# Optimization experiments

Hardware: AMD Instinct MI355X
Metric: run time of the kernel (lower is better)

The kernel has to match this reference:

```python
import jax, jax.numpy as jnp
import numpy as np

EMBED_DIM = 768
NUM_HEADS = 12
HEAD_DIM = EMBED_DIM // NUM_HEADS


def setup_inputs() -> dict:
    key = jax.random.key(0)
    ks = jax.random.split(key, 5)
    B, N, D = 8, 1024, EMBED_DIM
    s = 1.0 / np.sqrt(D)
    return {
        "x": jax.random.normal(ks[0], (B, N, D), dtype=jnp.float32),
        "qkv_w": jax.random.uniform(ks[1], (D, 3 * D), jnp.float32, -s, s),  # [in, out]
        "qkv_b": jax.random.uniform(ks[2], (3 * D,), jnp.float32, -s, s),
        "proj_w": jax.random.uniform(ks[3], (D, D), jnp.float32, -s, s),
        "proj_b": jax.random.uniform(ks[4], (D,), jnp.float32, -s, s),
    }


def reference(x, qkv_w, qkv_b, proj_w, proj_b):
    B, N, D = x.shape
    H, Hd = NUM_HEADS, HEAD_DIM
    qkv = x @ qkv_w + qkv_b                          # [B, N, 3D]
    qkv = qkv.reshape(B, N, 3, H, Hd)
    q, k, v = (jnp.moveaxis(qkv, 2, 0)[i].transpose(0, 2, 1, 3) for i in range(3))  # each [B, H, N, Hd]
    scores = jnp.einsum("bhnd,bhmd->bhnm", q, k) / np.sqrt(Hd).astype(x.dtype)
    attn = jax.nn.softmax(scores, axis=-1)           # dropout rate 0.0 -> identity
    out = jnp.einsum("bhnm,bhmd->bhnd", attn, v)     # [B, H, N, Hd]
    out = out.transpose(0, 2, 1, 3).reshape(B, N, D)
    return out @ proj_w + proj_b
```

## Files before the change

### kernel.cpp

```cpp
#include <hip/hip_runtime.h>
#include <hip/hip_bf16.h>

typedef __attribute__((ext_vector_type(8))) short short8;
typedef __attribute__((ext_vector_type(4))) float f32x4;
typedef __attribute__((ext_vector_type(2))) unsigned int uint2v;
typedef unsigned int u32;

#define QSCALE 0.1803368801111204f

__device__ inline ushort f2bf(float f) {
    unsigned int i = __builtin_bit_cast(unsigned int, f);
    unsigned int r = (i + 0x7FFFu + ((i >> 16) & 1u)) >> 16;
    return (ushort)r;
}
__device__ inline u32 pack_bf16(float a, float b) {
    float2 f2; f2.x = a; f2.y = b;
    __hip_bfloat162 h = __float22bfloat162_rn(f2);
    u32 r; __builtin_memcpy(&r, &h, 4);
    return r;
}

__device__ __forceinline__ void gload_lds16(const ushort* g, ushort* l) {
    __builtin_amdgcn_global_load_lds(
        (const __attribute__((address_space(1))) u32*)g,
        (__attribute__((address_space(3))) u32*)l, 16, 0, 0);
}

__global__ __launch_bounds__(256) void convert_f32_bf16(
    const float* __restrict__ in, ushort* __restrict__ outp, int n8)
{
    int idx = blockIdx.x * 256 + threadIdx.x;
    if (idx >= n8) return;
    const float4 u0 = *(const float4*)&in[(size_t)idx * 8];
    const float4 u1 = *(const float4*)&in[(size_t)idx * 8 + 4];
    uint2v a, b;
    a.x = pack_bf16(u0.x, u0.y); a.y = pack_bf16(u0.z, u0.w);
    b.x = pack_bf16(u1.x, u1.y); b.y = pack_bf16(u1.z, u1.w);
    *(uint2v*)&outp[(size_t)idx * 8] = a;
    *(uint2v*)&outp[(size_t)idx * 8 + 4] = b;
}

__global__ __launch_bounds__(256) void transpose_f32_bf16(
    const float* __restrict__ W, ushort* __restrict__ Wt, int K, int N)
{
    __shared__ float tile[32][33];
    const int n0 = blockIdx.x * 32;
    const int k0 = blockIdx.y * 32;
    const int tx = threadIdx.x & 31;
    const int ty = threadIdx.x >> 5;
    for (int i = ty; i < 32; i += 8)
        tile[i][tx] = W[(size_t)(k0 + i) * N + n0 + tx];
    __syncthreads();
    for (int i = ty; i < 32; i += 8)
        Wt[(size_t)(n0 + i) * K + k0 + tx] = f2bf(tile[tx][i]);
}

template <bool OUT_FP32, bool QKV_MODE>
__global__ __launch_bounds__(256) void gemm_bt(
    const ushort* __restrict__ A, const ushort* __restrict__ Bt,
    const float* __restrict__ bias, void* __restrict__ C,
    ushort* __restrict__ Vt, int M, int N, int K, int ldc)
{
    __shared__ __attribute__((aligned(16))) ushort As[128][64];
    __shared__ __attribute__((aligned(16))) ushort Bs[128][64];
    const int tid  = threadIdx.x;
    const int lane = tid & 63;
    const int w    = tid >> 6;
    const int wm   = (w >> 1) * 64;
    const int wn   = (w & 1) * 64;
    const int g    = lane >> 4;
    const int t    = lane & 15;
    const int m0   = blockIdx.y * 128;
    const int n0   = blockIdx.x * 128;

    const int lr = lane >> 3;
    const int pc = lane & 7;

    f32x4 acc[4][4];
#pragma unroll
    for (int i = 0; i < 4; i++)
#pragma unroll
        for (int j = 0; j < 4; j++) acc[i][j] = {0.f, 0.f, 0.f, 0.f};

    const int xorc = t & 7;

    for (int k0 = 0; k0 < K; k0 += 64) {
#pragma unroll
        for (int p = 0; p < 4; p++) {
            const int row = w * 32 + p * 8 + lr;
            const int gc  = pc ^ (row & 7);
            gload_lds16(&A[(size_t)(m0 + row) * K + k0 + gc * 8], &As[w * 32 + p * 8][0]);
            gload_lds16(&Bt[(size_t)(n0 + row) * K + k0 + gc * 8], &Bs[w * 32 + p * 8][0]);
        }
        __syncthreads();
#pragma unroll
        for (int s = 0; s < 2; s++) {
            short8 a[4], b[4];
            const int ca = ((s * 4 + g) ^ xorc) * 8;
#pragma unroll
            for (int i = 0; i < 4; i++)
                a[i] = *(const short8*)&As[wm + i * 16 + t][ca];
#pragma unroll
            for (int j = 0; j < 4; j++)
                b[j] = *(const short8*)&Bs[wn + j * 16 + t][ca];
#pragma unroll
            for (int i = 0; i < 4; i++)
#pragma unroll
                for (int j = 0; j < 4; j++)
                    acc[i][j] = __builtin_amdgcn_mfma_f32_16x16x32_bf16(
                        a[i], b[j], acc[i][j], 0, 0, 0);
        }
        __syncthreads();
    }

#pragma unroll
    for (int j = 0; j < 4; j++) {
        int col = n0 + wn + j * 16 + t;
        float bv = bias[col];
        if (QKV_MODE && col >= 1536) {
            int h = (col - 1536) >> 6, d = col & 63;
#pragma unroll
            for (int i = 0; i < 4; i++) {
                int n = m0 + wm + i * 16 + g * 4;
                int bb = n >> 10, nn = n & 1023;
                uint2v u;
                u.x = pack_bf16(acc[i][j][0] + bv, acc[i][j][1] + bv);
                u.y = pack_bf16(acc[i][j][2] + bv, acc[i][j][3] + bv);
                *(uint2v*)&Vt[(((size_t)bb * 12 + h) * 64 + d) * 1024 + nn] = u;
            }
        } else {
#pragma unroll
            for (int i = 0; i < 4; i++)
#pragma unroll
                for (int r = 0; r < 4; r++) {
                    int row = m0 + wm + i * 16 + g * 4 + r;
                    float val = acc[i][j][r] + bv;
                    if (QKV_MODE && col < 768) val *= QSCALE;
                    if (OUT_FP32) ((float*)C)[(size_t)row * ldc + col] = val;
                    else          ((ushort*)C)[(size_t)row * ldc + col] = f2bf(val);
                }
        }
    }
}

#define PD 72
__global__ __launch_bounds__(256) void attn_kernel(
    const ushort* __restrict__ qk, const ushort* __restrict__ Vt,
    ushort* __restrict__ out)
{
    __shared__ __attribute__((aligned(16))) ushort Ks[2][64][64];
    __shared__ __attribute__((aligned(16))) ushort Vs[2][64][64];
    __shared__ __attribute__((aligned(16))) ushort Ps[4][16][PD];

    const int tid  = threadIdx.x;
    const int lane = tid & 63;
    const int w    = tid >> 6;
    const int g    = lane >> 4;
    const int t    = lane & 15;
    const int q0   = blockIdx.x * 128;
    const int h    = blockIdx.y;
    const int b    = blockIdx.z;

    const int srow = tid >> 3;
    const int pc   = tid & 7;
    const size_t base  = (size_t)b * 1024 * 1536;
    const size_t vbase = ((size_t)b * 12 + h) * 64 * 1024;

    short8 qfrag[2][2];
#pragma unroll
    for (int qf = 0; qf < 2; qf++)
#pragma unroll
        for (int s = 0; s < 2; s++)
            qfrag[qf][s] = *(const short8*)&qk[base +
                (size_t)(q0 + qf * 64 + w * 16 + t) * 1536 + h * 64 + s * 32 + g * 8];

#pragma unroll
    for (int p = 0; p < 2; p++) {
        int r = srow + 32 * p;
        int c = (pc ^ (r & 7)) * 8;
        *(short8*)&Ks[0][r][c] =
            *(const short8*)&qk[base + (size_t)r * 1536 + 768 + h * 64 + pc * 8];
        *(short8*)&Vs[0][r][c] =
            *(const short8*)&Vt[vbase + (size_t)r * 1024 + pc * 8];
    }
    __syncthreads();

    f32x4 o_acc[2][4];
#pragma unroll
    for (int qf = 0; qf < 2; qf++)
#pragma unroll
        for (int j = 0; j < 4; j++) o_acc[qf][j] = {0.f, 0.f, 0.f, 0.f};
    float l_part[2] = {0.f, 0.f};

    for (int kt = 0; kt < 16; kt++) {
        const int cur = kt & 1;

        short8 kpre[2], vpre[2];
        if (kt < 15) {
            const int kb = (kt + 1) * 64;
#pragma unroll
            for (int p = 0; p < 2; p++) {
                int r = srow + 32 * p;
                kpre[p] = *(const short8*)&qk[base + (size_t)(kb + r) * 1536 + 768 + h * 64 + pc * 8];
                vpre[p] = *(const short8*)&Vt[vbase + (size_t)r * 1024 + kb + pc * 8];
            }
        }

        short8 kf[2][4], bv[2][4];
#pragma unroll
        for (int s = 0; s < 2; s++)
#pragma unroll
            for (int j = 0; j < 4; j++) {
                const int row = j * 16 + t;
                const int c = ((s * 4 + g) ^ (t & 7)) * 8;
                kf[s][j] = *(const short8*)&Ks[cur][row][c];
                bv[s][j] = *(const short8*)&Vs[cur][row][c];
            }

#pragma unroll
        for (int qf = 0; qf < 2; qf++) {
            f32x4 s_acc[4];
#pragma unroll
            for (int j = 0; j < 4; j++) s_acc[j] = {0.f, 0.f, 0.f, 0.f};
#pragma unroll
            for (int s = 0; s < 2; s++)
#pragma unroll
                for (int j = 0; j < 4; j++)
                    s_acc[j] = __builtin_amdgcn_mfma_f32_16x16x32_bf16(
                        kf[s][j], qfrag[qf][s], s_acc[j], 0, 0, 0);

#pragma unroll
            for (int j = 0; j < 4; j++) {
                float p0 = exp2f(s_acc[j][0]);
                float p1 = exp2f(s_acc[j][1]);
                float p2 = exp2f(s_acc[j][2]);
                float p3 = exp2f(s_acc[j][3]);
                l_part[qf] += (p0 + p1) + (p2 + p3);
                uint2v u;
                u.x = pack_bf16(p0, p1);
                u.y = pack_bf16(p2, p3);
                *(uint2v*)&Ps[w][t][j * 16 + g * 4] = u;
            }

#pragma unroll
            for (int s = 0; s < 2; s++) {
                short8 a = *(const short8*)&Ps[w][t][s * 32 + g * 8];
#pragma unroll
                for (int j = 0; j < 4; j++)
                    o_acc[qf][j] = __builtin_amdgcn_mfma_f32_16x16x32_bf16(
                        a, bv[s][j], o_acc[qf][j], 0, 0, 0);
            }
        }

        if (kt < 15) {
#pragma unroll
            for (int p = 0; p < 2; p++) {
                int r = srow + 32 * p;
                int c = (pc ^ (r & 7)) * 8;
                *(short8*)&Ks[cur ^ 1][r][c] = kpre[p];
                *(short8*)&Vs[cur ^ 1][r][c] = vpre[p];
            }
        }
        __syncthreads();
    }

#pragma unroll
    for (int qf = 0; qf < 2; qf++) {
        float l_tot = l_part[qf];
        l_tot += __shfl_xor(l_tot, 16);
        l_tot += __shfl_xor(l_tot, 32);
        float il[4];
#pragma unroll
        for (int r = 0; r < 4; r++) il[r] = 1.0f / __shfl(l_tot, g * 4 + r);
#pragma unroll
        for (int r = 0; r < 4; r++) {
            int row = q0 + qf * 64 + w * 16 + g * 4 + r;
#pragma unroll
            for (int j = 0; j < 4; j++)
                out[((size_t)(b * 1024 + row)) * 768 + h * 64 + j * 16 + t] =
                    f2bf(o_acc[qf][j][r] * il[r]);
        }
    }
}

extern "C" void kernel_launch(void* const* d_in, const int* in_sizes, int n_in,
                              void* d_out, int out_size, void* d_ws, size_t ws_size,
                              hipStream_t stream)
{
    const float* x      = (const float*)d_in[0];
    const float* qkv_w  = (const float*)d_in[1];
    const float* qkv_b  = (const float*)d_in[2];
    const float* proj_w = (const float*)d_in[3];
    const float* proj_b = (const float*)d_in[4];
    float* out = (float*)d_out;

    char* ws = (char*)d_ws;
    ushort* Wt1 = (ushort*)ws;
    ushort* Wt2 = Wt1 + (size_t)2304 * 768;
    char*   buf = (char*)(Wt2 + (size_t)768 * 768);

    transpose_f32_bf16<<<dim3(72, 24), 256, 0, stream>>>(qkv_w, Wt1, 768, 2304);
    transpose_f32_bf16<<<dim3(24, 24), 256, 0, stream>>>(proj_w, Wt2, 768, 768);

    const size_t wt_bytes   = ((size_t)2304 * 768 + (size_t)768 * 768) * 2;
    const size_t full_bytes = wt_bytes + (size_t)8192 * 768 * 2
                                       + (size_t)8192 * 1536 * 2
                                       + (size_t)8192 * 768 * 2
                                       + (size_t)8192 * 768 * 2;

    if (ws_size >= full_bytes) {
        ushort* xb    = (ushort*)buf;
        ushort* qkO   = xb + (size_t)8192 * 768;
        ushort* VtO   = qkO + (size_t)8192 * 1536;
        ushort* attnO = VtO + (size_t)8192 * 768;
        convert_f32_bf16<<<dim3(3072), 256, 0, stream>>>(x, xb, 786432);
        gemm_bt<false, true><<<dim3(18, 64), 256, 0, stream>>>(
            xb, Wt1, qkv_b, qkO, VtO, 8192, 2304, 768, 1536);
        attn_kernel<<<dim3(8, 12, 8), 256, 0, stream>>>(qkO, VtO, attnO);
        gemm_bt<true, false><<<dim3(6, 64), 256, 0, stream>>>(
            attnO, Wt2, proj_b, out, nullptr, 8192, 768, 768, 768);
    } else {
        ushort* xbB   = (ushort*)buf;
        ushort* qkB   = xbB + (size_t)1024 * 768;
        ushort* VtB   = qkB + (size_t)1024 * 1536;
        ushort* attnB = VtB + (size_t)1024 * 768;
        for (int b = 0; b < 8; b++) {
            const float* xp = x + (size_t)b * 1024 * 768;
            float* outb = out + (size_t)b * 1024 * 768;
            convert_f32_bf16<<<dim3(384), 256, 0, stream>>>(xp, xbB, 98304);
            gemm_bt<false, true><<<dim3(18, 8), 256, 0, stream>>>(
                xbB, Wt1, qkv_b, qkB, VtB, 1024, 2304, 768, 1536);
            attn_kernel<<<dim3(8, 12, 1), 256, 0, stream>>>(qkB, VtB, attnB);
            gemm_bt<true, false><<<dim3(6, 8), 256, 0, stream>>>(
                attnB, Wt2, proj_b, outb, nullptr, 1024, 768, 768, 768);
        }
    }
}
```

Before: 207.8 us.

## Add 64x128-tile projection GEMM and single-buffer attention K/V LDS with register prefetch

Adds a dedicated output-projection GEMM that uses 64x128 tiles, which doubles the block count from 384 to 768 for better CU fill on the 8192x768 problem. The attention kernel moves from double-buffered K/V shared memory to a single buffer. It prefetches tiles two steps ahead in registers and adds an extra barrier per iteration. This cuts LDS use, which may raise occupancy, but it adds a sync and the prefetch distance changes.

```diff
diff --git a/kernel.cpp b/kernel.cpp
--- a/kernel.cpp
+++ b/kernel.cpp
@@ -143,13 +143,88 @@
     }
 }
 
+__global__ __launch_bounds__(256) void gemm_bt2(
+    const ushort* __restrict__ A, const ushort* __restrict__ Bt,
+    const float* __restrict__ bias, float* __restrict__ C,
+    int M, int N, int K, int ldc)
+{
+    __shared__ __attribute__((aligned(16))) ushort As[64][64];
+    __shared__ __attribute__((aligned(16))) ushort Bs[128][64];
+    const int tid  = threadIdx.x;
+    const int lane = tid & 63;
+    const int w    = tid >> 6;
+    const int g    = lane >> 4;
+    const int t    = lane & 15;
+    const int m0   = blockIdx.y * 64;
+    const int n0   = blockIdx.x * 128;
+    const int wn   = w * 32;
+
+    const int lr = lane >> 3;
+    const int pc = lane & 7;
+
+    f32x4 acc[4][2];
+#pragma unroll
+    for (int i = 0; i < 4; i++)
+#pragma unroll
+        for (int j = 0; j < 2; j++) acc[i][j] = {0.f, 0.f, 0.f, 0.f};
+
+    const int xorc = t & 7;
+
+    for (int k0 = 0; k0 < K; k0 += 64) {
+#pragma unroll
+        for (int p = 0; p < 2; p++) {
+            const int row = w * 16 + p * 8 + lr;
+            const int gc  = pc ^ (row & 7);
+            gload_lds16(&A[(size_t)(m0 + row) * K + k0 + gc * 8], &As[w * 16 + p * 8][0]);
+        }
+#pragma unroll
+        for (int p = 0; p < 4; p++) {
+            const int row = w * 32 + p * 8 + lr;
+            const int gc  = pc ^ (row & 7);
+            gload_lds16(&Bt[(size_t)(n0 + row) * K + k0 + gc * 8], &Bs[w * 32 + p * 8][0]);
+        }
+        __syncthreads();
+#pragma unroll
+        for (int s = 0; s < 2; s++) {
+            short8 a[4], b[2];
+            const int ca = ((s * 4 + g) ^ xorc) * 8;
+#pragma unroll
+            for (int i = 0; i < 4; i++)
+                a[i] = *(const short8*)&As[i * 16 + t][ca];
+#pragma unroll
+            for (int j = 0; j < 2; j++)
+                b[j] = *(const short8*)&Bs[wn + j * 16 + t][ca];
+#pragma unroll
+            for (int i = 0; i < 4; i++)
+#pragma unroll
+                for (int j = 0; j < 2; j++)
+                    acc[i][j] = __builtin_amdgcn_mfma_f32_16x16x32_bf16(
+                        a[i], b[j], acc[i][j], 0, 0, 0);
+        }
+        __syncthreads();
+    }
+
+#pragma unroll
+    for (int j = 0; j < 2; j++) {
+        int col = n0 + wn + j * 16 + t;
+        float bv = bias[col];
+#pragma unroll
+        for (int i = 0; i < 4; i++)
+#pragma unroll
+            for (int r = 0; r < 4; r++) {
+                int row = m0 + i * 16 + g * 4 + r;
+                C[(size_t)row * ldc + col] = acc[i][j][r] + bv;
+            }
+    }
+}
+
 #define PD 72
 __global__ __launch_bounds__(256) void attn_kernel(
     const ushort* __restrict__ qk, const ushort* __restrict__ Vt,
     ushort* __restrict__ out)
 {
-    __shared__ __attribute__((aligned(16))) ushort Ks[2][64][64];
-    __shared__ __attribute__((aligned(16))) ushort Vs[2][64][64];
+    __shared__ __attribute__((aligned(16))) ushort Ks[64][64];
+    __shared__ __attribute__((aligned(16))) ushort Vs[64][64];
     __shared__ __attribute__((aligned(16))) ushort Ps[4][16][PD];
 
     const int tid  = threadIdx.x;
@@ -178,10 +253,17 @@
     for (int p = 0; p < 2; p++) {
         int r = srow + 32 * p;
         int c = (pc ^ (r & 7)) * 8;
-        *(short8*)&Ks[0][r][c] =
+        *(short8*)&Ks[r][c] =
             *(const short8*)&qk[base + (size_t)r * 1536 + 768 + h * 64 + pc * 8];
-        *(short8*)&Vs[0][r][c] =
+        *(short8*)&Vs[r][c] =
             *(const short8*)&Vt[vbase + (size_t)r * 1024 + pc * 8];
+    }
+    short8 kpre[2], vpre[2];
+#pragma unroll
+    for (int p = 0; p < 2; p++) {
+        int r = srow + 32 * p;
+        kpre[p] = *(const short8*)&qk[base + (size_t)(64 + r) * 1536 + 768 + h * 64 + pc * 8];
+        vpre[p] = *(const short8*)&Vt[vbase + (size_t)r * 1024 + 64 + pc * 8];
     }
     __syncthreads();
 
@@ -193,19 +275,6 @@
     float l_part[2] = {0.f, 0.f};
 
     for (int kt = 0; kt < 16; kt++) {
-        const int cur = kt & 1;
-
-        short8 kpre[2], vpre[2];
-        if (kt < 15) {
-            const int kb = (kt + 1) * 64;
-#pragma unroll
-            for (int p = 0; p < 2; p++) {
-                int r = srow + 32 * p;
-                kpre[p] = *(const short8*)&qk[base + (size_t)(kb + r) * 1536 + 768 + h * 64 + pc * 8];
-                vpre[p] = *(const short8*)&Vt[vbase + (size_t)r * 1024 + kb + pc * 8];
-            }
-        }
-
         short8 kf[2][4], bv[2][4];
 #pragma unroll
         for (int s = 0; s < 2; s++)
@@ -213,9 +282,29 @@
             for (int j = 0; j < 4; j++) {
                 const int row = j * 16 + t;
                 const int c = ((s * 4 + g) ^ (t & 7)) * 8;
-                kf[s][j] = *(const short8*)&Ks[cur][row][c];
-                bv[s][j] = *(const short8*)&Vs[cur][row][c];
-            }
+                kf[s][j] = *(const short8*)&Ks[row][c];
+                bv[s][j] = *(const short8*)&Vs[row][c];
+            }
+        __syncthreads();
+
+        if (kt < 15) {
+#pragma unroll
+            for (int p = 0; p < 2; p++) {
+                int r = srow + 32 * p;
+                int c = (pc ^ (r & 7)) * 8;
+                *(short8*)&Ks[r][c] = kpre[p];
+                *(short8*)&Vs[r][c] = vpre[p];
+            }
+            if (kt < 14) {
+                const int kb = (kt + 2) * 64;
+#pragma unroll
+                for (int p = 0; p < 2; p++) {
+                    int r = srow + 32 * p;
+                    kpre[p] = *(const short8*)&qk[base + (size_t)(kb + r) * 1536 + 768 + h * 64 + pc * 8];
+                    vpre[p] = *(const short8*)&Vt[vbase + (size_t)r * 1024 + kb + pc * 8];
+                }
+            }
+        }
 
 #pragma unroll
         for (int qf = 0; qf < 2; qf++) {
@@ -251,16 +340,6 @@
                         a, bv[s][j], o_acc[qf][j], 0, 0, 0);
             }
         }
-
-        if (kt < 15) {
-#pragma unroll
-            for (int p = 0; p < 2; p++) {
-                int r = srow + 32 * p;
-                int c = (pc ^ (r & 7)) * 8;
-                *(short8*)&Ks[cur ^ 1][r][c] = kpre[p];
-                *(short8*)&Vs[cur ^ 1][r][c] = vpre[p];
-            }
-        }
         __syncthreads();
     }
 
@@ -317,8 +396,8 @@
         gemm_bt<false, true><<<dim3(18, 64), 256, 0, stream>>>(
             xb, Wt1, qkv_b, qkO, VtO, 8192, 2304, 768, 1536);
         attn_kernel<<<dim3(8, 12, 8), 256, 0, stream>>>(qkO, VtO, attnO);
-        gemm_bt<true, false><<<dim3(6, 64), 256, 0, stream>>>(
-            attnO, Wt2, proj_b, out, nullptr, 8192, 768, 768, 768);
+        gemm_bt2<<<dim3(6, 128), 256, 0, stream>>>(
+            attnO, Wt2, proj_b, out, 8192, 768, 768, 768);
     } else {
         ushort* xbB   = (ushort*)buf;
         ushort* qkB   = xbB + (size_t)1024 * 768;
@@ -331,8 +410,8 @@
             gemm_bt<false, true><<<dim3(18, 8), 256, 0, stream>>>(
                 xbB, Wt1, qkv_b, qkB, VtB, 1024, 2304, 768, 1536);
             attn_kernel<<<dim3(8, 12, 1), 256, 0, stream>>>(qkB, VtB, attnB);
-            gemm_bt<true, false><<<dim3(6, 8), 256, 0, stream>>>(
-                attnB, Wt2, proj_b, outb, nullptr, 1024, 768, 768, 768);
-        }
-    }
-}
+            gemm_bt2<<<dim3(6, 16), 256, 0, stream>>>(
+                attnB, Wt2, proj_b, outb, 1024, 768, 768, 768);
+        }
+    }
+}
```

Result: no change. 209.1 us (+0.7%).
